# Kernel tuning notes

Hardware: AMD Instinct MI355X
Metric: run time of the kernel (lower is better)

The kernel has to match this reference:

```python
import jax, jax.numpy as jnp
import numpy as np

WH, WW = 7, 7
N = WH * WW
HEADS = 12
HEAD_DIM = 16
EMBED = 384
INNER = HEADS * HEAD_DIM
NW = 64
B_ = 2048
SCALE = HEAD_DIM ** -0.5


def _relative_position_index():
    ch, cw = np.meshgrid(np.arange(WH), np.arange(WW), indexing='ij')
    coords = np.stack([ch.ravel(), cw.ravel()])              # [2, N]
    rel = coords[:, :, None] - coords[:, None, :]             # [2, N, N]
    rel = rel.transpose(1, 2, 0)
    rel[:, :, 0] += WH - 1
    rel[:, :, 1] += WW - 1
    rel[:, :, 0] *= 2 * WW - 1
    return jnp.asarray(rel.sum(-1), dtype=jnp.int32)          # [N, N]


def setup_inputs() -> dict:
    key = jax.random.key(0)
    ks = jax.random.split(key, 8)
    s_in = EMBED ** -0.5
    s_inner = INNER ** -0.5
    x = jax.random.normal(ks[0], (B_, N, EMBED), jnp.float32)
    # Swin shift mask: 0 or -100 per window pair
    mbits = jax.random.bernoulli(ks[1], 0.2, (NW, N, N))
    mask = jnp.where(mbits, jnp.float32(-100.0), jnp.float32(0.0))
    return {
        'x': x,
        'mask': mask,
        'Wq': jax.random.normal(ks[2], (EMBED, INNER), jnp.float32) * s_in,
        'bq': jnp.zeros((INNER,), jnp.float32),
        'Wk': jax.random.normal(ks[3], (EMBED, INNER), jnp.float32) * s_in,
        'bk': jnp.zeros((INNER,), jnp.float32),
        'Wv': jax.random.normal(ks[4], (EMBED, INNER), jnp.float32) * s_in,
        'bv': jnp.zeros((INNER,), jnp.float32),
        'Wp': jax.random.normal(ks[5], (INNER, EMBED), jnp.float32) * s_inner,
        'bp': jnp.zeros((EMBED,), jnp.float32),
        'bias_table': jax.random.normal(ks[6], ((2 * WH - 1) * (2 * WW - 1), HEADS), jnp.float32) * 0.02,
        'rel_idx': _relative_position_index(),
    }


def reference(x, mask, Wq, bq, Wk, bk, Wv, bv, Wp, bp, bias_table, rel_idx):
    B, n, _ = x.shape
    q = (x @ Wq + bq).reshape(B, n, HEADS, HEAD_DIM)
    k = (x @ Wk + bk).reshape(B, n, HEADS, HEAD_DIM)
    v = (x @ Wv + bv).reshape(B, n, HEADS, HEAD_DIM)
    attn = jnp.einsum('bnhd,bmhd->bhnm', q * SCALE, k)        # [B, H, N, N]
    bias = bias_table[rel_idx]                                 # [N, N, H]
    attn = attn + jnp.transpose(bias, (2, 0, 1))[None]
    nW = mask.shape[0]
    attn = attn.reshape(B // nW, nW, HEADS, n, n) + mask[None, :, None]
    attn = jax.nn.softmax(attn.reshape(B, HEADS, n, n), axis=-1)
    out = jnp.einsum('bhnm,bmhd->bnhd', attn, v).reshape(B, n, INNER)
    return out @ Wp + bp
```

## Files before the change

kernel.cpp:

```cpp
#include <hip/hip_runtime.h>


typedef __attribute__((ext_vector_type(8))) short  bf8;
typedef __attribute__((ext_vector_type(4))) short  bf4;
typedef __attribute__((ext_vector_type(4))) float  f4;

union B8 { bf8 v; unsigned u[4]; };

__device__ __forceinline__ short f2b(float f) {
  unsigned u = __builtin_bit_cast(unsigned, f);
  unsigned r = u + 0x7fffu + ((u >> 16) & 1u);
  return (short)(r >> 16);
}
__device__ __forceinline__ unsigned pk2(float lo, float hi) {
  return (unsigned)(unsigned short)f2b(lo) | ((unsigned)(unsigned short)f2b(hi) << 16);
}
__device__ __forceinline__ float b2f(unsigned short b) {
  return __builtin_bit_cast(float, (unsigned)b << 16);
}
__device__ __forceinline__ unsigned dperm(int addr, unsigned lo, unsigned hi, bool glo) {
  int a = __builtin_amdgcn_ds_bpermute(addr, (int)lo);
  int b = __builtin_amdgcn_ds_bpermute(addr, (int)hi);
  return (unsigned)(glo ? a : b);
}

__global__ void wa_prep(const float* __restrict__ Wq, const float* __restrict__ Wk,
                        const float* __restrict__ Wv, const float* __restrict__ Wp,
                        const float* __restrict__ btab, const int* __restrict__ ridx,
                        const float* __restrict__ mask,
                        short* __restrict__ wt, short* __restrict__ wpt,
                        unsigned short* __restrict__ biasS, unsigned short* __restrict__ maskS) {
  int id = blockIdx.x * 256 + threadIdx.x;
  const int NWT = 576 * 384, NWP = 384 * 192, NBS = 12 * 64 * 64, NMS = 64 * 64 * 64;
  if (id < NWT) {
    int row = id / 384, k = id - row * 384;
    int kind = row / 192, cc = row - kind * 192;
    const float* W = (kind == 0) ? Wq : (kind == 1 ? Wk : Wv);
    float v = W[k * 192 + cc];
    if (kind == 0) v *= 0.25f;
    wt[id] = f2b(v);
  } else if ((id -= NWT) < NWP) {
    int n = id / 192, k = id - n * 192;
    wpt[id] = f2b(Wp[k * 384 + n]);
  } else if ((id -= NWP) < NBS) {
    int h = id >> 12, rem = id & 4095;
    int n = rem >> 6, cc = rem & 63;
    int m = (cc & 3) * 16 + (cc >> 2);
    float v;
    if (n >= 49)      v = -10000.0f;
    else if (m >= 49) v = 0.0f;
    else              v = btab[ridx[m * 49 + n] * 12 + h];
    biasS[id] = (unsigned short)f2b(v);
  } else if ((id -= NBS) < NMS) {
    int win = id >> 12, rem = id & 4095;
    int n = rem >> 6, cc = rem & 63;
    int m = (cc & 3) * 16 + (cc >> 2);
    float v = (m < 49 && n < 49) ? mask[win * 2401 + m * 49 + n] : 0.f;
    maskS[id] = (unsigned short)f2b(v);
  }
}

struct __align__(16) Smem {
  union U {
    short xs[64][392];
    struct QK { short qs[64][200]; short ks[64][200]; } qk;
  } u;
};

__global__ __launch_bounds__(256, 2)
void wa_main(const float* __restrict__ x,
             const float* __restrict__ bq, const float* __restrict__ bk,
             const float* __restrict__ bv, const float* __restrict__ bp,
             const short* __restrict__ wt, const short* __restrict__ wpt,
             const unsigned short* __restrict__ biasS, const unsigned short* __restrict__ maskS,
             float* __restrict__ out) {
  __shared__ Smem sm;
  const int tid = threadIdx.x;
  const int w   = tid >> 6;
  const int lid = tid & 63;
  const int g   = lid >> 4;
  const int c   = lid & 15;
  const int blk = blockIdx.x;
  const int mwin = (blk & 63) << 12;

  {
    const float* xw = x + (size_t)blk * 18816;
    f4 xv[18];
#pragma unroll
    for (int it = 0; it < 18; it++) {
      int i = tid + it * 256;
      xv[it] = *(const f4*)(xw + (i / 96) * 384 + (i % 96) * 4);
    }
    const int iT = tid + 18 * 256;
    f4 xt = {0.f, 0.f, 0.f, 0.f};
    if (iT < 4704) xt = *(const f4*)(xw + (iT / 96) * 384 + (iT % 96) * 4);
#pragma unroll
    for (int it = 0; it < 18; it++) {
      int i = tid + it * 256;
      bf4 pk = {f2b(xv[it][0]), f2b(xv[it][1]), f2b(xv[it][2]), f2b(xv[it][3])};
      *(bf4*)&sm.u.xs[i / 96][(i % 96) * 4] = pk;
    }
    if (iT < 4704) {
      bf4 pk = {f2b(xt[0]), f2b(xt[1]), f2b(xt[2]), f2b(xt[3])};
      *(bf4*)&sm.u.xs[iT / 96][(iT % 96) * 4] = pk;
    }
    const bf8 zz = {0,0,0,0,0,0,0,0};
#pragma unroll
    for (int it = 0; it < 3; it++) {
      int i = tid + it * 256;
      if (i < 735) { int row = 49 + i / 49, c8 = (i % 49) * 8; *(bf8*)&sm.u.xs[row][c8] = zz; }
    }
  }
  __syncthreads();

  f4 acc[4][9];
#pragma unroll
  for (int mt = 0; mt < 4; mt++)
#pragma unroll
    for (int i = 0; i < 9; i++) acc[mt][i] = (f4){0.f, 0.f, 0.f, 0.f};
  int rowb[9];
#pragma unroll
  for (int i = 0; i < 9; i++) {
    int kind = i / 3, hh = 3 * w + i % 3;
    rowb[i] = (kind * 192 + hh * 16 + c) * 384;
  }
#pragma unroll 3
  for (int ks = 0; ks < 12; ks++) {
    const int k0 = ks * 32 + g * 8;
    bf8 a[4], b[9];
#pragma unroll
    for (int mt = 0; mt < 4; mt++) a[mt] = *(const bf8*)&sm.u.xs[mt * 16 + c][k0];
#pragma unroll
    for (int i = 0; i < 9; i++) b[i] = *(const bf8*)(wt + rowb[i] + k0);
#pragma unroll
    for (int mt = 0; mt < 4; mt++)
#pragma unroll
      for (int i = 0; i < 9; i++)
        acc[mt][i] = __builtin_amdgcn_mfma_f32_16x16x32_bf16(a[mt], b[i], acc[mt][i], 0, 0, 0);
  }
  __syncthreads();

  unsigned vpk[3][4][2];
#pragma unroll
  for (int i = 0; i < 9; i++) {
    const int kind = i / 3, hh = 3 * w + i % 3;
    const int col = hh * 16 + c;
    const float bb = (kind == 0) ? 0.25f * bq[col] : (kind == 1 ? bk[col] : bv[col]);
#pragma unroll
    for (int mt = 0; mt < 4; mt++) {
      if (kind == 2) {
        vpk[i - 6][mt][0] = pk2(acc[mt][i][0] + bb, acc[mt][i][1] + bb);
        vpk[i - 6][mt][1] = pk2(acc[mt][i][2] + bb, acc[mt][i][3] + bb);
      } else {
        short* dst = (kind == 0) ? &sm.u.qk.qs[0][0] : &sm.u.qk.ks[0][0];
#pragma unroll
        for (int r = 0; r < 4; r++)
          dst[(mt * 16 + g * 4 + r) * 200 + col] = f2b(acc[mt][i][r] + bb);
      }
    }
  }
  asm volatile("" ::: "memory");

  const int  addrA = c * 4 + (((2 * g)     & 3) << 6);
  const int  addrB = c * 4 + (((2 * g + 1) & 3) << 6);
  const bool glo   = (g < 2);
  const f4   z4 = {0.f, 0.f, 0.f, 0.f};
  const bf8  z8 = {0,0,0,0,0,0,0,0};
#pragma unroll
  for (int t = 0; t < 3; t++) {
    const int h  = 3 * w + t;
    const int hb = h * 16;
    bf8 afr[4], bfr[4];
#pragma unroll
    for (int nt = 0; nt < 4; nt++)
      afr[nt] = glo ? *(const bf8*)&sm.u.qk.ks[nt * 16 + c][hb + g * 8] : z8;
#pragma unroll
    for (int mt = 0; mt < 4; mt++)
      bfr[mt] = glo ? *(const bf8*)&sm.u.qk.qs[mt * 16 + c][hb + g * 8] : z8;
    f4 s[4][4];
#pragma unroll
    for (int nt = 0; nt < 4; nt++)
#pragma unroll
      for (int mt = 0; mt < 4; mt++)
        s[nt][mt] = __builtin_amdgcn_mfma_f32_16x16x32_bf16(afr[nt], bfr[mt], z4, 0, 0, 0);
    const unsigned short* bsH = biasS + (h << 12);
#pragma unroll
    for (int nt = 0; nt < 4; nt++)
#pragma unroll
      for (int r = 0; r < 4; r++) {
        const int n = nt * 16 + g * 4 + r;
        bf4 b4 = *(const bf4*)&bsH[n * 64 + c * 4];
        bf4 m4 = *(const bf4*)&maskS[mwin + n * 64 + c * 4];
#pragma unroll
        for (int mt = 0; mt < 4; mt++)
          s[nt][mt][r] += b2f((unsigned short)b4[mt]) + b2f((unsigned short)m4[mt]);
      }
#pragma unroll
    for (int mt = 0; mt < 4; mt++) {
      float mx = -3e38f;
#pragma unroll
      for (int nt = 0; nt < 4; nt++)
#pragma unroll
        for (int r = 0; r < 4; r++) mx = fmaxf(mx, s[nt][mt][r]);
      mx = fmaxf(mx, __shfl_xor(mx, 16, 64));
      mx = fmaxf(mx, __shfl_xor(mx, 32, 64));
      float sum = 0.f;
#pragma unroll
      for (int nt = 0; nt < 4; nt++)
#pragma unroll
        for (int r = 0; r < 4; r++) {
          float p = __expf(s[nt][mt][r] - mx);
          s[nt][mt][r] = p;
          sum += p;
        }
      sum += __shfl_xor(sum, 16, 64);
      sum += __shfl_xor(sum, 32, 64);
      const float rinv = 1.f / sum;
#pragma unroll
      for (int nt = 0; nt < 4; nt++)
#pragma unroll
        for (int r = 0; r < 4; r++) s[nt][mt][r] *= rinv;
    }
    unsigned ppk[4][4][2];
#pragma unroll
    for (int nt = 0; nt < 4; nt++)
#pragma unroll
      for (int mt = 0; mt < 4; mt++) {
        ppk[nt][mt][0] = pk2(s[nt][mt][0], s[nt][mt][1]);
        ppk[nt][mt][1] = pk2(s[nt][mt][2], s[nt][mt][3]);
      }
    f4 o[4];
#pragma unroll
    for (int mt = 0; mt < 4; mt++) o[mt] = z4;
#pragma unroll
    for (int ks2 = 0; ks2 < 2; ks2++) {
      B8 va;
      va.u[0] = dperm(addrA, vpk[t][2 * ks2][0], vpk[t][2 * ks2 + 1][0], glo);
      va.u[1] = dperm(addrA, vpk[t][2 * ks2][1], vpk[t][2 * ks2 + 1][1], glo);
      va.u[2] = dperm(addrB, vpk[t][2 * ks2][0], vpk[t][2 * ks2 + 1][0], glo);
      va.u[3] = dperm(addrB, vpk[t][2 * ks2][1], vpk[t][2 * ks2 + 1][1], glo);
#pragma unroll
      for (int mt = 0; mt < 4; mt++) {
        B8 pb;
        pb.u[0] = dperm(addrA, ppk[2 * ks2][mt][0], ppk[2 * ks2 + 1][mt][0], glo);
        pb.u[1] = dperm(addrA, ppk[2 * ks2][mt][1], ppk[2 * ks2 + 1][mt][1], glo);
        pb.u[2] = dperm(addrB, ppk[2 * ks2][mt][0], ppk[2 * ks2 + 1][mt][0], glo);
        pb.u[3] = dperm(addrB, ppk[2 * ks2][mt][1], ppk[2 * ks2 + 1][mt][1], glo);
        o[mt] = __builtin_amdgcn_mfma_f32_16x16x32_bf16(va.v, pb.v, o[mt], 0, 0, 0);
      }
    }
#pragma unroll
    for (int mt = 0; mt < 4; mt++) {
      bf4 pk = {f2b(o[mt][0]), f2b(o[mt][1]), f2b(o[mt][2]), f2b(o[mt][3])};
      *(bf4*)&sm.u.qk.qs[mt * 16 + c][hb + g * 4] = pk;
    }
    asm volatile("" ::: "memory");
  }
  __syncthreads();

  f4 acc3[6][4];
#pragma unroll
  for (int jt = 0; jt < 6; jt++)
#pragma unroll
    for (int mt = 0; mt < 4; mt++) acc3[jt][mt] = z4;
#pragma unroll 2
  for (int ks3 = 0; ks3 < 6; ks3++) {
    const int k0 = ks3 * 32 + g * 8;
    bf8 ao[4], wb[6];
#pragma unroll
    for (int mt = 0; mt < 4; mt++) ao[mt] = *(const bf8*)&sm.u.qk.qs[mt * 16 + c][k0];
#pragma unroll
    for (int jt = 0; jt < 6; jt++)
      wb[jt] = *(const bf8*)(wpt + (w * 96 + jt * 16 + c) * 192 + k0);
#pragma unroll
    for (int jt = 0; jt < 6; jt++)
#pragma unroll
      for (int mt = 0; mt < 4; mt++)
        acc3[jt][mt] = __builtin_amdgcn_mfma_f32_16x16x32_bf16(wb[jt], ao[mt], acc3[jt][mt], 0, 0, 0);
  }
  float* ow = out + (size_t)blk * 18816;
#pragma unroll
  for (int jt = 0; jt < 6; jt++) {
    const int colb = w * 96 + jt * 16 + g * 4;
    const f4 bp4 = *(const f4*)&bp[colb];
#pragma unroll
    for (int mt = 0; mt < 4; mt++) {
      const int m = mt * 16 + c;
      if (m < 49) {
        f4 v = acc3[jt][mt] + bp4;
        *(f4*)&ow[m * 384 + colb] = v;
      }
    }
  }
}

extern "C" void kernel_launch(void* const* d_in, const int* in_sizes, int n_in,
                              void* d_out, int out_size, void* d_ws, size_t ws_size,
                              hipStream_t stream) {
  const float* x    = (const float*)d_in[0];
  const float* mask = (const float*)d_in[1];
  const float* Wq   = (const float*)d_in[2];
  const float* bq   = (const float*)d_in[3];
  const float* Wk   = (const float*)d_in[4];
  const float* bk   = (const float*)d_in[5];
  const float* Wv   = (const float*)d_in[6];
  const float* bv   = (const float*)d_in[7];
  const float* Wp   = (const float*)d_in[8];
  const float* bp   = (const float*)d_in[9];
  const float* btab = (const float*)d_in[10];
  const int*   ridx = (const int*)d_in[11];
  float* out = (float*)d_out;

  char* ws = (char*)d_ws;
  short* wt            = (short*)ws;
  short* wpt           = (short*)(ws + 442368);
  unsigned short* biasS = (unsigned short*)(ws + 589824);
  unsigned short* maskS = (unsigned short*)(ws + 688128);

  wa_prep<<<dim3(2368), dim3(256), 0, stream>>>(Wq, Wk, Wv, Wp, btab, ridx, mask,
                                                wt, wpt, biasS, maskS);
  wa_main<<<dim3(2048), dim3(256), 0, stream>>>(x, bq, bk, bv, bp, wt, wpt, biasS, maskS, out);
}
```

Before: 234.9 us.

## Split QKV projection into QK and V passes to raise occupancy

Splits the fused 9-tile QKV GEMM into a Q/K pass with 6 accumulator tiles and a separate V pass with 3 tiles. Q/K results are packed to bf16 in registers and written to shared memory after the barrier. This cuts peak accumulator register pressure, and the launch bounds move from 2 to 3 blocks per SM. The cost is reading the x tile from LDS twice, plus extra loop overhead and possible spills if the compiler cannot fit 3 blocks.

```diff
diff --git a/kernel.cpp b/kernel.cpp
--- a/kernel.cpp
+++ b/kernel.cpp
@@ -67,7 +67,7 @@
   } u;
 };
 
-__global__ __launch_bounds__(256, 2)
+__global__ __launch_bounds__(256, 3)
 void wa_main(const float* __restrict__ x,
              const float* __restrict__ bq, const float* __restrict__ bk,
              const float* __restrict__ bv, const float* __restrict__ bp,
@@ -113,51 +113,95 @@
   }
   __syncthreads();
 
-  f4 acc[4][9];
-#pragma unroll
-  for (int mt = 0; mt < 4; mt++)
-#pragma unroll
-    for (int i = 0; i < 9; i++) acc[mt][i] = (f4){0.f, 0.f, 0.f, 0.f};
-  int rowb[9];
-#pragma unroll
-  for (int i = 0; i < 9; i++) {
-    int kind = i / 3, hh = 3 * w + i % 3;
-    rowb[i] = (kind * 192 + hh * 16 + c) * 384;
-  }
+  unsigned qpk[3][4][2], kpk[3][4][2];
+  {
+    f4 accA[4][6];
+#pragma unroll
+    for (int mt = 0; mt < 4; mt++)
+#pragma unroll
+      for (int i = 0; i < 6; i++) accA[mt][i] = (f4){0.f, 0.f, 0.f, 0.f};
+    int rqk[6];
+#pragma unroll
+    for (int i = 0; i < 6; i++)
+      rqk[i] = ((i / 3) * 192 + (3 * w + i % 3) * 16 + c) * 384;
 #pragma unroll 3
-  for (int ks = 0; ks < 12; ks++) {
-    const int k0 = ks * 32 + g * 8;
-    bf8 a[4], b[9];
-#pragma unroll
-    for (int mt = 0; mt < 4; mt++) a[mt] = *(const bf8*)&sm.u.xs[mt * 16 + c][k0];
-#pragma unroll
-    for (int i = 0; i < 9; i++) b[i] = *(const bf8*)(wt + rowb[i] + k0);
+    for (int ks = 0; ks < 12; ks++) {
+      const int k0 = ks * 32 + g * 8;
+      bf8 a[4], b[6];
+#pragma unroll
+      for (int mt = 0; mt < 4; mt++) a[mt] = *(const bf8*)&sm.u.xs[mt * 16 + c][k0];
+#pragma unroll
+      for (int i = 0; i < 6; i++) b[i] = *(const bf8*)(wt + rqk[i] + k0);
+#pragma unroll
+      for (int mt = 0; mt < 4; mt++)
+#pragma unroll
+        for (int i = 0; i < 6; i++)
+          accA[mt][i] = __builtin_amdgcn_mfma_f32_16x16x32_bf16(a[mt], b[i], accA[mt][i], 0, 0, 0);
+    }
+#pragma unroll
+    for (int i = 0; i < 3; i++) {
+      const int col = (3 * w + i) * 16 + c;
+      const float bqv = 0.25f * bq[col], bkv = bk[col];
+#pragma unroll
+      for (int mt = 0; mt < 4; mt++) {
+        qpk[i][mt][0] = pk2(accA[mt][i][0] + bqv, accA[mt][i][1] + bqv);
+        qpk[i][mt][1] = pk2(accA[mt][i][2] + bqv, accA[mt][i][3] + bqv);
+        kpk[i][mt][0] = pk2(accA[mt][3 + i][0] + bkv, accA[mt][3 + i][1] + bkv);
+        kpk[i][mt][1] = pk2(accA[mt][3 + i][2] + bkv, accA[mt][3 + i][3] + bkv);
+      }
+    }
+  }
+
+  unsigned vpk[3][4][2];
+  {
+    f4 accB[4][3];
 #pragma unroll
     for (int mt = 0; mt < 4; mt++)
 #pragma unroll
-      for (int i = 0; i < 9; i++)
-        acc[mt][i] = __builtin_amdgcn_mfma_f32_16x16x32_bf16(a[mt], b[i], acc[mt][i], 0, 0, 0);
+      for (int i = 0; i < 3; i++) accB[mt][i] = (f4){0.f, 0.f, 0.f, 0.f};
+    int rv[3];
+#pragma unroll
+    for (int i = 0; i < 3; i++) rv[i] = (384 + (3 * w + i) * 16 + c) * 384;
+#pragma unroll 3
+    for (int ks = 0; ks < 12; ks++) {
+      const int k0 = ks * 32 + g * 8;
+      bf8 a[4], b[3];
+#pragma unroll
+      for (int mt = 0; mt < 4; mt++) a[mt] = *(const bf8*)&sm.u.xs[mt * 16 + c][k0];
+#pragma unroll
+      for (int i = 0; i < 3; i++) b[i] = *(const bf8*)(wt + rv[i] + k0);
+#pragma unroll
+      for (int mt = 0; mt < 4; mt++)
+#pragma unroll
+        for (int i = 0; i < 3; i++)
+          accB[mt][i] = __builtin_amdgcn_mfma_f32_16x16x32_bf16(a[mt], b[i], accB[mt][i], 0, 0, 0);
+    }
+#pragma unroll
+    for (int i = 0; i < 3; i++) {
+      const int col = (3 * w + i) * 16 + c;
+      const float bvv = bv[col];
+#pragma unroll
+      for (int mt = 0; mt < 4; mt++) {
+        vpk[i][mt][0] = pk2(accB[mt][i][0] + bvv, accB[mt][i][1] + bvv);
+        vpk[i][mt][1] = pk2(accB[mt][i][2] + bvv, accB[mt][i][3] + bvv);
+      }
+    }
   }
   __syncthreads();
 
-  unsigned vpk[3][4][2];
-#pragma unroll
-  for (int i = 0; i < 9; i++) {
-    const int kind = i / 3, hh = 3 * w + i % 3;
-    const int col = hh * 16 + c;
-    const float bb = (kind == 0) ? 0.25f * bq[col] : (kind == 1 ? bk[col] : bv[col]);
-#pragma unroll
-    for (int mt = 0; mt < 4; mt++) {
-      if (kind == 2) {
-        vpk[i - 6][mt][0] = pk2(acc[mt][i][0] + bb, acc[mt][i][1] + bb);
-        vpk[i - 6][mt][1] = pk2(acc[mt][i][2] + bb, acc[mt][i][3] + bb);
-      } else {
-        short* dst = (kind == 0) ? &sm.u.qk.qs[0][0] : &sm.u.qk.ks[0][0];
-#pragma unroll
-        for (int r = 0; r < 4; r++)
-          dst[(mt * 16 + g * 4 + r) * 200 + col] = f2b(acc[mt][i][r] + bb);
-      }
-    }
+#pragma unroll
+  for (int i = 0; i < 3; i++) {
+    const int col = (3 * w + i) * 16 + c;
+#pragma unroll
+    for (int mt = 0; mt < 4; mt++)
+#pragma unroll
+      for (int rp = 0; rp < 2; rp++) {
+        unsigned qv = qpk[i][mt][rp], kv = kpk[i][mt][rp];
+        sm.u.qk.qs[mt * 16 + g * 4 + 2 * rp][col]     = (short)(qv & 0xFFFFu);
+        sm.u.qk.qs[mt * 16 + g * 4 + 2 * rp + 1][col] = (short)(qv >> 16);
+        sm.u.qk.ks[mt * 16 + g * 4 + 2 * rp][col]     = (short)(kv & 0xFFFFu);
+        sm.u.qk.ks[mt * 16 + g * 4 + 2 * rp + 1][col] = (short)(kv >> 16);
+      }
   }
   asm volatile("" ::: "memory");
 
```

Result: slower. 272.7 us (+16.1%).

## Split QKV projection into per-kind passes to cut registers and raise occupancy

Applied to the files above, without the earlier changes.

The single QKV GEMM loop kept 36 f4 accumulators live. It is replaced by six smaller passes (Q, K, V, each over two halves of the row tiles) that hold only 6 accumulators at a time and pack results to bf16 in registers. Launch bounds are raised from 2 to 3 blocks per SIMD to use the lower register pressure for occupancy. The cost is that each x tile is re-read from LDS three times and each weight tile twice. The packed Q/K values are also kept in registers until the final LDS write, which may offset some of the register savings.

```diff
diff --git a/kernel.cpp b/kernel.cpp
--- a/kernel.cpp
+++ b/kernel.cpp
@@ -67,7 +67,43 @@
   } u;
 };
 
-__global__ __launch_bounds__(256, 2)
+#define QKV_PASS(ROWOFF, BIASEXPR, DST)                                        \
+  _Pragma("unroll")                                                            \
+  for (int mth = 0; mth < 2; mth++) {                                          \
+    f4 acc[2][3];                                                              \
+    _Pragma("unroll")                                                          \
+    for (int m2 = 0; m2 < 2; m2++)                                             \
+      _Pragma("unroll")                                                        \
+      for (int i = 0; i < 3; i++) acc[m2][i] = (f4){0.f, 0.f, 0.f, 0.f};       \
+    _Pragma("unroll 3")                                                        \
+    for (int ks = 0; ks < 12; ks++) {                                          \
+      const int k0 = ks * 32 + g * 8;                                          \
+      bf8 a[2], b[3];                                                          \
+      _Pragma("unroll")                                                        \
+      for (int m2 = 0; m2 < 2; m2++)                                           \
+        a[m2] = *(const bf8*)&sm.u.xs[(mth * 2 + m2) * 16 + c][k0];            \
+      _Pragma("unroll")                                                        \
+      for (int i = 0; i < 3; i++)                                              \
+        b[i] = *(const bf8*)(wt + ((ROWOFF) + (3 * w + i) * 16 + c) * 384 + k0); \
+      _Pragma("unroll")                                                        \
+      for (int m2 = 0; m2 < 2; m2++)                                           \
+        _Pragma("unroll")                                                      \
+        for (int i = 0; i < 3; i++)                                            \
+          acc[m2][i] = __builtin_amdgcn_mfma_f32_16x16x32_bf16(a[m2], b[i], acc[m2][i], 0, 0, 0); \
+    }                                                                          \
+    _Pragma("unroll")                                                          \
+    for (int i = 0; i < 3; i++) {                                              \
+      const int col = (3 * w + i) * 16 + c;                                    \
+      const float bb = (BIASEXPR);                                             \
+      _Pragma("unroll")                                                        \
+      for (int m2 = 0; m2 < 2; m2++) {                                         \
+        DST[i][mth * 2 + m2][0] = pk2(acc[m2][i][0] + bb, acc[m2][i][1] + bb); \
+        DST[i][mth * 2 + m2][1] = pk2(acc[m2][i][2] + bb, acc[m2][i][3] + bb); \
+      }                                                                        \
+    }                                                                          \
+  }
+
+__global__ __launch_bounds__(256, 3)
 void wa_main(const float* __restrict__ x,
              const float* __restrict__ bq, const float* __restrict__ bk,
              const float* __restrict__ bv, const float* __restrict__ bp,
@@ -113,51 +149,25 @@
   }
   __syncthreads();
 
-  f4 acc[4][9];
-#pragma unroll
-  for (int mt = 0; mt < 4; mt++)
-#pragma unroll
-    for (int i = 0; i < 9; i++) acc[mt][i] = (f4){0.f, 0.f, 0.f, 0.f};
-  int rowb[9];
-#pragma unroll
-  for (int i = 0; i < 9; i++) {
-    int kind = i / 3, hh = 3 * w + i % 3;
-    rowb[i] = (kind * 192 + hh * 16 + c) * 384;
-  }
-#pragma unroll 3
-  for (int ks = 0; ks < 12; ks++) {
-    const int k0 = ks * 32 + g * 8;
-    bf8 a[4], b[9];
-#pragma unroll
-    for (int mt = 0; mt < 4; mt++) a[mt] = *(const bf8*)&sm.u.xs[mt * 16 + c][k0];
-#pragma unroll
-    for (int i = 0; i < 9; i++) b[i] = *(const bf8*)(wt + rowb[i] + k0);
+  unsigned qpk[3][4][2], kpk[3][4][2], vpk[3][4][2];
+  QKV_PASS(0,   0.25f * bq[col], qpk)
+  QKV_PASS(192, bk[col],         kpk)
+  QKV_PASS(384, bv[col],         vpk)
+  __syncthreads();
+
+#pragma unroll
+  for (int i = 0; i < 3; i++) {
+    const int col = (3 * w + i) * 16 + c;
 #pragma unroll
     for (int mt = 0; mt < 4; mt++)
 #pragma unroll
-      for (int i = 0; i < 9; i++)
-        acc[mt][i] = __builtin_amdgcn_mfma_f32_16x16x32_bf16(a[mt], b[i], acc[mt][i], 0, 0, 0);
-  }
-  __syncthreads();
-
-  unsigned vpk[3][4][2];
-#pragma unroll
-  for (int i = 0; i < 9; i++) {
-    const int kind = i / 3, hh = 3 * w + i % 3;
-    const int col = hh * 16 + c;
-    const float bb = (kind == 0) ? 0.25f * bq[col] : (kind == 1 ? bk[col] : bv[col]);
-#pragma unroll
-    for (int mt = 0; mt < 4; mt++) {
-      if (kind == 2) {
-        vpk[i - 6][mt][0] = pk2(acc[mt][i][0] + bb, acc[mt][i][1] + bb);
-        vpk[i - 6][mt][1] = pk2(acc[mt][i][2] + bb, acc[mt][i][3] + bb);
-      } else {
-        short* dst = (kind == 0) ? &sm.u.qk.qs[0][0] : &sm.u.qk.ks[0][0];
-#pragma unroll
-        for (int r = 0; r < 4; r++)
-          dst[(mt * 16 + g * 4 + r) * 200 + col] = f2b(acc[mt][i][r] + bb);
-      }
-    }
+      for (int rp = 0; rp < 2; rp++) {
+        unsigned qv = qpk[i][mt][rp], kv = kpk[i][mt][rp];
+        sm.u.qk.qs[mt * 16 + g * 4 + 2 * rp][col]     = (short)(qv & 0xFFFFu);
+        sm.u.qk.qs[mt * 16 + g * 4 + 2 * rp + 1][col] = (short)(qv >> 16);
+        sm.u.qk.ks[mt * 16 + g * 4 + 2 * rp][col]     = (short)(kv & 0xFFFFu);
+        sm.u.qk.ks[mt * 16 + g * 4 + 2 * rp + 1][col] = (short)(kv >> 16);
+      }
   }
   asm volatile("" ::: "memory");
 
```

New measurement: 361.8 us. +54.0%, slower.
